# Optimization experiments

Hardware: AMD Instinct MI355X
Metric: run time of the kernel (lower is better)

Reference implementation:

```python
import jax, jax.numpy as jnp
import numpy as np

B, T, C = 1024, 2048, 5
DTHETA = 0.15
EPS_W = 1e-6
EPS_SQRT = 1e-12  # tiny stabilizer inside sqrt (dx==0 at t=0 column)


def compute_paths(p, dtheta=DTHETA):
    """p: [B, T, 5] per-step (soft) one-hot action weights.
    Returns (px, py): [B, T+1] integrated path coordinates.
    Faithful to the torch nested-loop recurrence:
      w = p/(p+1e-6); fw = w0+w3+w4; dth = dtheta*(w1-w2+w3-w4)
      x += fw*cos(theta); y += fw*sin(theta); theta += dth (theta read before update)
    """
    w = p / (p + EPS_W)                               # [B,T,5]
    fw = w[..., 0] + w[..., 3] + w[..., 4]            # [B,T]
    dth = dtheta * (w[..., 1] - w[..., 2] + w[..., 3] - w[..., 4])  # [B,T]
    bsz = p.shape[0]
    z = jnp.zeros((bsz,), p.dtype)

    def step(carry, inp):
        x, y, th = carry
        f, d = inp
        nx = x + f * jnp.cos(th)
        ny = y + f * jnp.sin(th)
        return (nx, ny, th + d), (nx, ny)

    _, (xs, ys) = jax.lax.scan(step, (z, z, z), (fw.T, dth.T))  # xs,ys: [T,B]
    zero_col = jnp.zeros((bsz, 1), p.dtype)
    px = jnp.concatenate([zero_col, xs.T], axis=1)    # [B,T+1]
    py = jnp.concatenate([zero_col, ys.T], axis=1)
    return px, py


def setup_inputs() -> dict:
    key = jax.random.key(0)
    k1, k2 = jax.random.split(key)
    outputs = jax.random.normal(k1, (B, T, C), dtype=jnp.float32)
    labels = jax.random.randint(k2, (B, T), 0, C, dtype=jnp.int64)
    return {"outputs": outputs, "labels": labels, "save": 123}


def reference(outputs, labels, save):
    # hard-argmax mask times softmax (mask built from .data -> constant)
    predicted = jnp.argmax(outputs, axis=2)
    mask = jax.nn.one_hot(predicted, C, dtype=outputs.dtype)
    soft_predictions = jax.nn.softmax(outputs, axis=2) * mask
    px_p, py_p = compute_paths(soft_predictions)
    true_onehot = jax.nn.one_hot(labels, C, dtype=outputs.dtype)
    px_t, py_t = compute_paths(true_onehot)
    dx = px_p - px_t
    # NOTE: original torch code uses the x-difference twice (its bug); kept faithful.
    loss = jnp.sqrt(dx * dx + dx * dx + EPS_SQRT).mean()
    return loss
```

## Files before the change

kernel.cpp:

```cpp
#include <hip/hip_runtime.h>
#include <math.h>

#define NT 512
#define WAVES (NT / 64)
#define T_DIM 2048
#define B_DIM 1024
#define CHUNK 4

typedef float f4 __attribute__((ext_vector_type(4)));
typedef int   i4 __attribute__((ext_vector_type(4)));

__device__ __forceinline__ int   biti(float x) { return __builtin_bit_cast(int, x); }
__device__ __forceinline__ float bitf(int x)   { return __builtin_bit_cast(float, x); }

__device__ __forceinline__ float wave_scan_dpp(float x) {
  x += bitf(__builtin_amdgcn_update_dpp(0, biti(x), 0x111, 0xf, 0xf, false));
  x += bitf(__builtin_amdgcn_update_dpp(0, biti(x), 0x112, 0xf, 0xf, false));
  x += bitf(__builtin_amdgcn_update_dpp(0, biti(x), 0x114, 0xf, 0xf, false));
  x += bitf(__builtin_amdgcn_update_dpp(0, biti(x), 0x118, 0xf, 0xf, false));
  x += bitf(__builtin_amdgcn_update_dpp(0, biti(x), 0x142, 0xa, 0xf, false));
  x += bitf(__builtin_amdgcn_update_dpp(0, biti(x), 0x143, 0xc, 0xf, false));
  return x;
}

__global__ __launch_bounds__(NT) void path_loss_rows(
    const float* __restrict__ outs,
    const int*   __restrict__ labels,
    float*       __restrict__ partial)
{
  __shared__ float2 wsum[WAVES];
  __shared__ float2 wsum2[WAVES];
  __shared__ float  rsum[WAVES];

  const int tid  = threadIdx.x;
  const int lane = tid & 63;
  const int wid  = tid >> 6;
  const int b    = blockIdx.x;
  const int t0   = tid * CHUNK;

  const float* rowO = outs   + (size_t)b * T_DIM * 5;
  const int*   rowL = labels + (size_t)b * T_DIM;

  float vals[20];
  const f4* vp = (const f4*)(rowO + (size_t)t0 * 5);
  #pragma unroll
  for (int j = 0; j < 5; ++j) {
    f4 v = vp[j];
    vals[4*j+0] = v[0]; vals[4*j+1] = v[1]; vals[4*j+2] = v[2]; vals[4*j+3] = v[3];
  }
  i4 lv = ((const i4*)rowL)[tid];
  int lbl[CHUNK] = { lv[0], lv[1], lv[2], lv[3] };

  const float WT = (float)(1.0 / (1.0 + 1e-6));
  float dthP[CHUNK], fwP[CHUNK], dthT[CHUNK], fwT[CHUNK];
  #pragma unroll
  for (int k = 0; k < CHUNK; ++k) {
    float o0 = vals[5*k+0], o1 = vals[5*k+1], o2 = vals[5*k+2],
          o3 = vals[5*k+3], o4 = vals[5*k+4];
    float m = o0; int am = 0;
    if (o1 > m) { m = o1; am = 1; }
    if (o2 > m) { m = o2; am = 2; }
    if (o3 > m) { m = o3; am = 3; }
    if (o4 > m) { m = o4; am = 4; }
    float sum = __expf(o0-m) + __expf(o1-m) + __expf(o2-m)
              + __expf(o3-m) + __expf(o4-m);
    float w = __builtin_amdgcn_rcpf(1.0f + 1e-6f * sum);
    float w15 = 0.15f * w;
    fwP[k]  = (am==0 || am==3 || am==4) ? w : 0.0f;
    dthP[k] = (am==1 || am==3) ? w15 : ((am==2 || am==4) ? -w15 : 0.0f);

    int l = lbl[k];
    fwT[k]  = (l==0 || l==3 || l==4) ? WT : 0.0f;
    dthT[k] = (l==1 || l==3) ? 0.15f*WT : ((l==2 || l==4) ? -0.15f*WT : 0.0f);
  }

  float2 csum = make_float2(0.f, 0.f);
  #pragma unroll
  for (int k = 0; k < CHUNK; ++k) { csum.x += dthP[k]; csum.y += dthT[k]; }

  float ix = wave_scan_dpp(csum.x);
  float iy = wave_scan_dpp(csum.y);
  if (lane == 63) wsum[wid] = make_float2(ix, iy);
  __syncthreads();
  float2 base = make_float2(0.f, 0.f);
  #pragma unroll
  for (int w = 0; w < WAVES; ++w) {
    float2 t = wsum[w];
    if (w < wid) { base.x += t.x; base.y += t.y; }
  }
  float thP = base.x + (ix - csum.x);
  float thT = base.y + (iy - csum.y);

  float cP[CHUNK], cT[CHUNK];
  float2 xsum = make_float2(0.f, 0.f);
  #pragma unroll
  for (int k = 0; k < CHUNK; ++k) {
    cP[k] = fwP[k] * __cosf(thP);
    cT[k] = fwT[k] * __cosf(thT);
    thP += dthP[k]; thT += dthT[k];
    xsum.x += cP[k]; xsum.y += cT[k];
  }

  float jx = wave_scan_dpp(xsum.x);
  float jy = wave_scan_dpp(xsum.y);
  if (lane == 63) wsum2[wid] = make_float2(jx, jy);
  __syncthreads();
  float2 base2 = make_float2(0.f, 0.f);
  #pragma unroll
  for (int w = 0; w < WAVES; ++w) {
    float2 t = wsum2[w];
    if (w < wid) { base2.x += t.x; base2.y += t.y; }
  }
  float xP = base2.x + (jx - xsum.x);
  float xT = base2.y + (jy - xsum.y);

  float acc = 0.f;
  #pragma unroll
  for (int k = 0; k < CHUNK; ++k) {
    xP += cP[k]; xT += cT[k];
    float dx = xP - xT;
    acc += __builtin_amdgcn_sqrtf(2.0f * dx * dx + 1e-12f);
  }

  float atot = wave_scan_dpp(acc);
  if (lane == 63) rsum[wid] = atot;
  __syncthreads();
  if (tid == 0) {
    float s = 0.f;
    #pragma unroll
    for (int w = 0; w < WAVES; ++w) s += rsum[w];
    partial[b] = s;
  }
}

__global__ __launch_bounds__(256) void path_loss_reduce(
    const float* __restrict__ partial, float* __restrict__ out)
{
  __shared__ double rb[4];
  const int tid = threadIdx.x, lane = tid & 63, wid = tid >> 6;
  f4 v = ((const f4*)partial)[tid];
  double s = (double)v[0] + (double)v[1] + (double)v[2] + (double)v[3];
  #pragma unroll
  for (int d = 32; d > 0; d >>= 1) s += __shfl_down(s, d, 64);
  if (lane == 0) rb[wid] = s;
  __syncthreads();
  if (tid == 0) {
    double tot = rb[0] + rb[1] + rb[2] + rb[3];
    tot += (double)B_DIM * 1e-6;
    out[0] = (float)(tot / ((double)B_DIM * (double)(T_DIM + 1)));
  }
}

extern "C" void kernel_launch(void* const* d_in, const int* in_sizes, int n_in,
                              void* d_out, int out_size, void* d_ws, size_t ws_size,
                              hipStream_t stream) {
  const float* outs   = (const float*)d_in[0];
  const int*   labels = (const int*)d_in[1];
  float* partial = (float*)d_ws;
  float* out     = (float*)d_out;

  path_loss_rows<<<B_DIM, NT, 0, stream>>>(outs, labels, partial);
  path_loss_reduce<<<1, 256, 0, stream>>>(partial, out);
}
```

Before: 16.28 us.

## Track heading as packed integer step counts and drop softmax exponentials

The per-step angle increments are replaced by small integer counts (offset by 2 so they stay non-negative), with predicted and true counts packed into one int. A single integer DPP wave scan then replaces the two float scans, and theta is rebuilt as 0.15 times the count. The softmax exp/rcp work is removed by treating the soft weight p/(p+1e-6) as exactly 1. This cuts ALU and transcendental work and one scan, but drops the ~1e-6 relative weight correction and relies on the packed 16-bit fields not overflowing for T=2048.

```diff
diff --git a/kernel.cpp b/kernel.cpp
--- a/kernel.cpp
+++ b/kernel.cpp
@@ -22,13 +22,22 @@
   x += bitf(__builtin_amdgcn_update_dpp(0, biti(x), 0x143, 0xc, 0xf, false));
   return x;
 }
+__device__ __forceinline__ int wave_scan_dpp_i(int x) {
+  x += __builtin_amdgcn_update_dpp(0, x, 0x111, 0xf, 0xf, false);
+  x += __builtin_amdgcn_update_dpp(0, x, 0x112, 0xf, 0xf, false);
+  x += __builtin_amdgcn_update_dpp(0, x, 0x114, 0xf, 0xf, false);
+  x += __builtin_amdgcn_update_dpp(0, x, 0x118, 0xf, 0xf, false);
+  x += __builtin_amdgcn_update_dpp(0, x, 0x142, 0xa, 0xf, false);
+  x += __builtin_amdgcn_update_dpp(0, x, 0x143, 0xc, 0xf, false);
+  return x;
+}
 
 __global__ __launch_bounds__(NT) void path_loss_rows(
     const float* __restrict__ outs,
     const int*   __restrict__ labels,
     float*       __restrict__ partial)
 {
-  __shared__ float2 wsum[WAVES];
+  __shared__ int    wsumI[WAVES];
   __shared__ float2 wsum2[WAVES];
   __shared__ float  rsum[WAVES];
 
@@ -51,8 +60,7 @@
   i4 lv = ((const i4*)rowL)[tid];
   int lbl[CHUNK] = { lv[0], lv[1], lv[2], lv[3] };
 
-  const float WT = (float)(1.0 / (1.0 + 1e-6));
-  float dthP[CHUNK], fwP[CHUNK], dthT[CHUNK], fwT[CHUNK];
+  int fwPb[CHUNK], fwTb[CHUNK], inc[CHUNK];
   #pragma unroll
   for (int k = 0; k < CHUNK; ++k) {
     float o0 = vals[5*k+0], o1 = vals[5*k+1], o2 = vals[5*k+2],
@@ -62,43 +70,40 @@
     if (o2 > m) { m = o2; am = 2; }
     if (o3 > m) { m = o3; am = 3; }
     if (o4 > m) { m = o4; am = 4; }
-    float sum = __expf(o0-m) + __expf(o1-m) + __expf(o2-m)
-              + __expf(o3-m) + __expf(o4-m);
-    float w = __builtin_amdgcn_rcpf(1.0f + 1e-6f * sum);
-    float w15 = 0.15f * w;
-    fwP[k]  = (am==0 || am==3 || am==4) ? w : 0.0f;
-    dthP[k] = (am==1 || am==3) ? w15 : ((am==2 || am==4) ? -w15 : 0.0f);
+    fwPb[k]  = (0b11001 >> am) & 1;
+    int incP = 2 + ((0b01010 >> am) & 1) - ((0b10100 >> am) & 1);
 
     int l = lbl[k];
-    fwT[k]  = (l==0 || l==3 || l==4) ? WT : 0.0f;
-    dthT[k] = (l==1 || l==3) ? 0.15f*WT : ((l==2 || l==4) ? -0.15f*WT : 0.0f);
+    fwTb[k]  = (0b11001 >> l) & 1;
+    int incT = 2 + ((0b01010 >> l) & 1) - ((0b10100 >> l) & 1);
+    inc[k] = incP | (incT << 16);
   }
 
-  float2 csum = make_float2(0.f, 0.f);
-  #pragma unroll
-  for (int k = 0; k < CHUNK; ++k) { csum.x += dthP[k]; csum.y += dthT[k]; }
-
-  float ix = wave_scan_dpp(csum.x);
-  float iy = wave_scan_dpp(csum.y);
-  if (lane == 63) wsum[wid] = make_float2(ix, iy);
+  int isum = inc[0] + inc[1] + inc[2] + inc[3];
+  int iincl = wave_scan_dpp_i(isum);
+  if (lane == 63) wsumI[wid] = iincl;
   __syncthreads();
-  float2 base = make_float2(0.f, 0.f);
+  int ibase = 0;
   #pragma unroll
   for (int w = 0; w < WAVES; ++w) {
-    float2 t = wsum[w];
-    if (w < wid) { base.x += t.x; base.y += t.y; }
+    int t = wsumI[w];
+    if (w < wid) ibase += t;
   }
-  float thP = base.x + (ix - csum.x);
-  float thT = base.y + (iy - csum.y);
+  int r = ibase + (iincl - isum);
 
   float cP[CHUNK], cT[CHUNK];
   float2 xsum = make_float2(0.f, 0.f);
+  const int tb2 = 2 * t0;
   #pragma unroll
   for (int k = 0; k < CHUNK; ++k) {
-    cP[k] = fwP[k] * __cosf(thP);
-    cT[k] = fwT[k] * __cosf(thT);
-    thP += dthP[k]; thT += dthT[k];
+    int nP = (r & 0xffff) - (tb2 + 2*k);
+    int nT = (r >> 16)    - (tb2 + 2*k);
+    float cp = __cosf(0.15f * (float)nP);
+    float ct = __cosf(0.15f * (float)nT);
+    cP[k] = fwPb[k] ? cp : 0.f;
+    cT[k] = fwTb[k] ? ct : 0.f;
     xsum.x += cP[k]; xsum.y += cT[k];
+    r += inc[k];
   }
 
   float jx = wave_scan_dpp(xsum.x);
```

Measured after the change: 15.86 us. -2.6%, faster.
